# Kernel optimization log

Measured on AMD Instinct MI355X. Metric: run time of the kernel, lower is better.

## Reference

```python
import jax, jax.numpy as jnp
import numpy as np

THRESHOLD = 1e-3  # hardcoded `thresholds = 0.001` in the sparse branch


def setup_inputs() -> dict:
    key = jax.random.key(0)
    k1, k2, k3, k4, k5 = jax.random.split(key, 5)
    b, r, d_in, d_out = 8, 4096, 768, 768
    x = jax.random.normal(k1, (b, r, d_in), dtype=jnp.float32)
    weight = jax.random.normal(k2, (d_out, d_in), dtype=jnp.float32) * 0.02
    bias = jax.random.normal(k3, (d_out,), dtype=jnp.float32) * 0.02
    U = jax.random.normal(k4, (d_in, d_in), dtype=jnp.float32) * (d_in ** -0.5)
    VT = jax.random.normal(k5, (d_out, d_out), dtype=jnp.float32) * (d_out ** -0.5)
    return {"x": x, "weight": weight, "bias": bias, "U": U, "VT": VT}


def reference(x, weight, bias, U, VT):
    # Sparse path (len_grads >= 30) of LinearFunctionSparseGrad.forward.
    # h = x @ U.T, rotated into the gradient basis.  [b, r, c]
    h = jnp.einsum('brc,dc->brd', x, U)
    # Threshold-sparsify: zero entries with |h| <= 0.001.
    h = jnp.where(jnp.abs(h) > THRESHOLD, h, jnp.zeros((), h.dtype))
    # Original: gather nonzero rows/cols, h[rows][:, cols] @ weight.T[cols],
    # then scatter back via I[:, rows] @ res_. Dropped cols are exactly-zero
    # columns and dropped rows are exactly-zero rows, so the math equals a
    # dense matmul on the masked tensor (no [b*r, b*r] identity needed).
    res = jnp.einsum('brc,oc->bro', h, weight)        # h @ weight.T
    res = jnp.einsum('bro,po->brp', res, VT)          # res_ @ VT.T (self.VT=VT_orig.T => VT here)
    return res + bias
```

## Files before the change

### kernel.cpp

```cpp
#include <hip/hip_runtime.h>
#include <hip/hip_bf16.h>

typedef __bf16 bf16_t;
typedef bf16_t bf16x8 __attribute__((ext_vector_type(8)));
typedef bf16_t bf16x4 __attribute__((ext_vector_type(4)));
typedef float  f32x4  __attribute__((ext_vector_type(4)));

#define BM 256
#define BN 128
#define BK 32
#define ABUF (BM * BK)
#define BBUF (BN * BK)

enum { EPI_NONE = 0, EPI_THRESH = 1, EPI_BIAS = 2 };

__device__ __forceinline__ void memfence() { asm volatile("" ::: "memory"); }
__device__ __forceinline__ void blockbar() {
    memfence(); __builtin_amdgcn_s_barrier(); memfence();
}

#define GLD16(src, dst) __builtin_amdgcn_global_load_lds( \
    (const __attribute__((address_space(1))) void*)(src), \
    (__attribute__((address_space(3))) void*)(dst), 16, 0, 0)

template <int EPI, typename CT>
__device__ __forceinline__
void gemm_tile(const bf16_t* __restrict__ A, const bf16_t* __restrict__ B,
               CT* __restrict__ C, const float* __restrict__ bias,
               int m0, int n0, int N, int K,
               bf16_t* __restrict__ As, bf16_t* __restrict__ Bs)
{
    const int lane = threadIdx.x & 63;
    const int wave = threadIdx.x >> 6;
    const int wm = wave >> 1;
    const int wn = wave & 1;

    const int fm   = lane & 15;
    const int q    = lane >> 4;
    const int fsw2 = (fm ^ (fm >> 2)) & 3;

    const int NT = K / BK;

    const bf16_t* ga0; const bf16_t* ga1; const bf16_t* gb;
    {
        const int u0 = (wave * 2) * 64 + lane;
        const int r0 = u0 >> 2;
        ga0 = A + (size_t)(m0 + r0) * K + (((u0 & 3) ^ ((r0 ^ (r0 >> 2)) & 3)) * 8);
        const int u1 = (wave * 2 + 1) * 64 + lane;
        const int r1 = u1 >> 2;
        ga1 = A + (size_t)(m0 + r1) * K + (((u1 & 3) ^ ((r1 ^ (r1 >> 2)) & 3)) * 8);
        const int ub = wave * 64 + lane;
        const int rb = ub >> 2;
        gb  = B + (size_t)(n0 + rb) * K + (((ub & 3) ^ ((rb ^ (rb >> 2)) & 3)) * 8);
    }
    const int la0 = wave * 1024;
    const int la1 = wave * 1024 + 512;
    const int lb  = wave * 512;

#define STAGE(tt, Ad, Bd) do {                                   \
    GLD16(ga0 + (size_t)(tt) * BK, (Ad) + la0);                  \
    GLD16(ga1 + (size_t)(tt) * BK, (Ad) + la1);                  \
    GLD16(gb  + (size_t)(tt) * BK, (Bd) + lb);                   \
} while (0)

    f32x4 acc[4][4];
#pragma unroll
    for (int i = 0; i < 4; ++i)
#pragma unroll
        for (int j = 0; j < 4; ++j) acc[i][j] = (f32x4){0.f, 0.f, 0.f, 0.f};

    STAGE(0, As, Bs);
    STAGE(1, As + ABUF, Bs + BBUF);
    asm volatile("s_waitcnt vmcnt(3)" ::: "memory");
    blockbar();

    int bc = 0;
    for (int t = 0; t < NT; ++t) {
        const bf16_t* __restrict__ Ab = As + bc * ABUF;
        const bf16_t* __restrict__ Bb = Bs + bc * BBUF;
        const int bs2 = (bc >= 1) ? bc - 1 : 2;
        const bool do_stage = (t + 2 < NT);

        bf16x8 af[4], bfr[4];
#pragma unroll
        for (int i = 0; i < 4; ++i) {
            const int row = wm * 64 + i * 16 + fm;
            af[i] = *(const bf16x8*)(Ab + (size_t)(row * 4 + (q ^ fsw2)) * 8);
        }
#pragma unroll
        for (int j = 0; j < 4; ++j) {
            const int row = wn * 64 + j * 16 + fm;
            bfr[j] = *(const bf16x8*)(Bb + (size_t)(row * 4 + (q ^ fsw2)) * 8);
        }
        if (do_stage) STAGE(t + 2, As + bs2 * ABUF, Bs + bs2 * BBUF);

        __builtin_amdgcn_s_setprio(1);
#pragma unroll
        for (int i = 0; i < 4; ++i)
#pragma unroll
            for (int j = 0; j < 4; ++j)
                acc[i][j] = __builtin_amdgcn_mfma_f32_16x16x32_bf16(
                    af[i], bfr[j], acc[i][j], 0, 0, 0);
        __builtin_amdgcn_s_setprio(0);

        if (t < NT - 1) {
            asm volatile("s_waitcnt lgkmcnt(0)" ::: "memory");
            if (do_stage) asm volatile("s_waitcnt vmcnt(3)" ::: "memory");
            else          asm volatile("s_waitcnt vmcnt(0)" ::: "memory");
            blockbar();
        }
        bc = (bc >= 2) ? 0 : bc + 1;
    }

#pragma unroll
    for (int i = 0; i < 4; ++i) {
#pragma unroll
        for (int j = 0; j < 4; ++j) {
            const int col = n0 + wn * 64 + j * 16 + fm;
            float bv = 0.f;
            if (EPI == EPI_BIAS) bv = bias[col];
#pragma unroll
            for (int r = 0; r < 4; ++r) {
                const int row = m0 + wm * 64 + i * 16 + q * 4 + r;
                float v = acc[i][j][r];
                if (EPI == EPI_THRESH) v = (fabsf(v) > 1e-3f) ? v : 0.f;
                if (EPI == EPI_BIAS) v += bv;
                C[(size_t)row * N + col] = (CT)v;
            }
        }
    }
#undef STAGE
}

__global__ __launch_bounds__(512, 4)
void gemm_h_wc(const bf16_t* __restrict__ xb, const bf16_t* __restrict__ Ub,
               bf16_t* __restrict__ h,
               const bf16_t* __restrict__ VTb, const bf16_t* __restrict__ Wt,
               bf16_t* __restrict__ Wc)
{
    __shared__ __align__(16) bf16_t As[3 * ABUF];
    __shared__ __align__(16) bf16_t Bs[3 * BBUF];
    const int b = blockIdx.x;
    if (b < 18) {
        gemm_tile<EPI_NONE, bf16_t>(VTb, Wt, Wc, nullptr,
                                    (b / 6) * BM, (b % 6) * BN, 768, 768, As, Bs);
    } else {
        const int bb = b - 18;
        const int L = (bb & 7) * 96 + (bb >> 3);
        gemm_tile<EPI_THRESH, bf16_t>(xb, Ub, h, nullptr,
                                      (L / 6) * BM, (L % 6) * BN, 768, 768, As, Bs);
    }
}

__global__ __launch_bounds__(512, 4)
void gemm_out(const bf16_t* __restrict__ h, const bf16_t* __restrict__ Wc,
              float* __restrict__ out, const float* __restrict__ bias)
{
    __shared__ __align__(16) bf16_t As[3 * ABUF];
    __shared__ __align__(16) bf16_t Bs[3 * BBUF];
    const int b = blockIdx.x;
    const int L = (b & 7) * 96 + (b >> 3);
    gemm_tile<EPI_BIAS, float>(h, Wc, out, bias,
                               (L / 6) * BM, (L % 6) * BN, 768, 768, As, Bs);
}

__global__ __launch_bounds__(256)
void prep(const float* __restrict__ x, const float* __restrict__ U,
          const float* __restrict__ VT, const float* __restrict__ w,
          bf16_t* __restrict__ xb, bf16_t* __restrict__ Ub,
          bf16_t* __restrict__ VTb, bf16_t* __restrict__ Wt)
{
    __shared__ float tt[32][33];
    const int b = blockIdx.x;
    if (b < 12864) {
        const float* src; bf16_t* dst; size_t e;
        if (b < 12288)      { src = x;  dst = xb;  e = (size_t)b * 2048; }
        else if (b < 12576) { src = U;  dst = Ub;  e = (size_t)(b - 12288) * 2048; }
        else                { src = VT; dst = VTb; e = (size_t)(b - 12576) * 2048; }
        const size_t i = e + (size_t)threadIdx.x * 8;
        const f32x4 v0 = *(const f32x4*)(src + i);
        const f32x4 v1 = *(const f32x4*)(src + i + 4);
        bf16x8 o;
        o[0] = (bf16_t)v0[0]; o[1] = (bf16_t)v0[1];
        o[2] = (bf16_t)v0[2]; o[3] = (bf16_t)v0[3];
        o[4] = (bf16_t)v1[0]; o[5] = (bf16_t)v1[1];
        o[6] = (bf16_t)v1[2]; o[7] = (bf16_t)v1[3];
        *(bf16x8*)(dst + i) = o;
    } else {
        const int t = b - 12864;
        const int bx = (t % 24) * 32, by = (t / 24) * 32;
        const int tx = threadIdx.x & 31, ty = threadIdx.x >> 5;
#pragma unroll
        for (int i = 0; i < 32; i += 8)
            tt[ty + i][tx] = w[(size_t)(by + ty + i) * 768 + bx + tx];
        __syncthreads();
#pragma unroll
        for (int i = 0; i < 32; i += 8)
            Wt[(size_t)(bx + ty + i) * 768 + by + tx] = (bf16_t)tt[tx][ty + i];
    }
}

extern "C" void kernel_launch(void* const* d_in, const int* in_sizes, int n_in,
                              void* d_out, int out_size, void* d_ws, size_t ws_size,
                              hipStream_t stream)
{
    const float* x    = (const float*)d_in[0];
    const float* w    = (const float*)d_in[1];
    const float* bias = (const float*)d_in[2];
    const float* U    = (const float*)d_in[3];
    const float* VT   = (const float*)d_in[4];
    float* out = (float*)d_out;

    const int D = 768;
    const int M = 8 * 4096;
    const size_t MD = (size_t)M * D;
    const size_t DD = (size_t)D * D;

    char* ws = (char*)d_ws;
    bf16_t* xb  = (bf16_t*)ws;
    bf16_t* h   = (bf16_t*)(ws + MD * 2);
    bf16_t* Ub  = (bf16_t*)(ws + MD * 4);
    bf16_t* VTb = (bf16_t*)(ws + MD * 4 + DD * 2);
    bf16_t* Wt  = (bf16_t*)(ws + MD * 4 + DD * 4);
    bf16_t* Wc  = (bf16_t*)(ws + MD * 4 + DD * 6);

    prep<<<13440, 256, 0, stream>>>(x, U, VT, w, xb, Ub, VTb, Wt);
    gemm_h_wc<<<18 + 768, 512, 0, stream>>>(xb, Ub, h, VTb, Wt, Wc);
    gemm_out<<<768, 512, 0, stream>>>(h, Wc, out, bias);
}
```

Before: 278.0 us.

## Fuse fp32-to-bf16 conversion of x into the first GEMM's LDS load path

Drops the separate prep pass that turned x into a bf16 copy. The first GEMM now streams fp32 x tiles straight into LDS and converts them to bf16 while loading MFMA fragments. This removes one full fp32 read plus a bf16 write and re-read of the large activation tensor. In exchange the A tile in LDS doubles in size (80KB of shared memory), the pipeline drops from three stages to two with full vmcnt(0) waits, and occupancy may fall.

Result: slower. 289.7 us (+4.2%).

```diff
diff --git a/kernel.cpp b/kernel.cpp
--- a/kernel.cpp
+++ b/kernel.cpp
@@ -132,23 +132,142 @@
 #undef STAGE
 }
 
+template <int EPI>
+__device__ __forceinline__
+void gemm_h_af32(const float* __restrict__ A, const bf16_t* __restrict__ B,
+                 bf16_t* __restrict__ C, int m0, int n0, int N, int K,
+                 float* __restrict__ As, bf16_t* __restrict__ Bs)
+{
+    const int lane = threadIdx.x & 63;
+    const int wave = threadIdx.x >> 6;
+    const int wm = wave >> 1;
+    const int wn = wave & 1;
+
+    const int fm   = lane & 15;
+    const int q    = lane >> 4;
+    const int fsw  = fm & 7;
+    const int fsw2 = (fm ^ (fm >> 2)) & 3;
+
+    const int NT = K / BK;
+
+    const float* gA0; const float* gA1; const float* gA2; const float* gA3;
+    {
+        const int u0 = (wave * 4 + 0) * 64 + lane; const int r0 = u0 >> 3;
+        gA0 = A + (size_t)(m0 + r0) * K + ((u0 & 7) ^ (r0 & 7)) * 4;
+        const int u1 = (wave * 4 + 1) * 64 + lane; const int r1 = u1 >> 3;
+        gA1 = A + (size_t)(m0 + r1) * K + ((u1 & 7) ^ (r1 & 7)) * 4;
+        const int u2 = (wave * 4 + 2) * 64 + lane; const int r2 = u2 >> 3;
+        gA2 = A + (size_t)(m0 + r2) * K + ((u2 & 7) ^ (r2 & 7)) * 4;
+        const int u3 = (wave * 4 + 3) * 64 + lane; const int r3 = u3 >> 3;
+        gA3 = A + (size_t)(m0 + r3) * K + ((u3 & 7) ^ (r3 & 7)) * 4;
+    }
+    const bf16_t* gb;
+    {
+        const int ub = wave * 64 + lane;
+        const int rb = ub >> 2;
+        gb = B + (size_t)(n0 + rb) * K + (((ub & 3) ^ ((rb ^ (rb >> 2)) & 3)) * 8);
+    }
+    const int lA = wave * 1024;
+    const int lb = wave * 512;
+
+#define HSTAGE(tt, Ad, Bd) do {                                  \
+    GLD16(gA0 + (size_t)(tt) * BK, (Ad) + lA);                   \
+    GLD16(gA1 + (size_t)(tt) * BK, (Ad) + lA + 256);             \
+    GLD16(gA2 + (size_t)(tt) * BK, (Ad) + lA + 512);             \
+    GLD16(gA3 + (size_t)(tt) * BK, (Ad) + lA + 768);             \
+    GLD16(gb  + (size_t)(tt) * BK, (Bd) + lb);                   \
+} while (0)
+
+    f32x4 acc[4][4];
+#pragma unroll
+    for (int i = 0; i < 4; ++i)
+#pragma unroll
+        for (int j = 0; j < 4; ++j) acc[i][j] = (f32x4){0.f, 0.f, 0.f, 0.f};
+
+    HSTAGE(0, As, Bs);
+    asm volatile("s_waitcnt vmcnt(0)" ::: "memory");
+    blockbar();
+
+    for (int t = 0; t < NT; ++t) {
+        const float*  __restrict__ Ab = As + (t & 1) * (BM * BK);
+        const bf16_t* __restrict__ Bb = Bs + (t & 1) * BBUF;
+
+        if (t + 1 < NT)
+            HSTAGE(t + 1, As + ((t + 1) & 1) * (BM * BK),
+                          Bs + ((t + 1) & 1) * BBUF);
+
+        bf16x8 af[4], bfr[4];
+#pragma unroll
+        for (int i = 0; i < 4; ++i) {
+            const int row = wm * 64 + i * 16 + fm;
+            const f32x4 lo = *(const f32x4*)(Ab + (size_t)(row * 8 + ((2 * q)     ^ fsw)) * 4);
+            const f32x4 hi = *(const f32x4*)(Ab + (size_t)(row * 8 + ((2 * q + 1) ^ fsw)) * 4);
+            bf16x8 v;
+            v[0] = (bf16_t)lo[0]; v[1] = (bf16_t)lo[1];
+            v[2] = (bf16_t)lo[2]; v[3] = (bf16_t)lo[3];
+            v[4] = (bf16_t)hi[0]; v[5] = (bf16_t)hi[1];
+            v[6] = (bf16_t)hi[2]; v[7] = (bf16_t)hi[3];
+            af[i] = v;
+        }
+#pragma unroll
+        for (int j = 0; j < 4; ++j) {
+            const int row = wn * 64 + j * 16 + fm;
+            bfr[j] = *(const bf16x8*)(Bb + (size_t)(row * 4 + (q ^ fsw2)) * 8);
+        }
+
+        __builtin_amdgcn_s_setprio(1);
+#pragma unroll
+        for (int i = 0; i < 4; ++i)
+#pragma unroll
+            for (int j = 0; j < 4; ++j)
+                acc[i][j] = __builtin_amdgcn_mfma_f32_16x16x32_bf16(
+                    af[i], bfr[j], acc[i][j], 0, 0, 0);
+        __builtin_amdgcn_s_setprio(0);
+
+        if (t < NT - 1) {
+            asm volatile("s_waitcnt lgkmcnt(0)" ::: "memory");
+            asm volatile("s_waitcnt vmcnt(0)" ::: "memory");
+            blockbar();
+        }
+    }
+
+#pragma unroll
+    for (int i = 0; i < 4; ++i) {
+#pragma unroll
+        for (int j = 0; j < 4; ++j) {
+            const int col = n0 + wn * 64 + j * 16 + fm;
+#pragma unroll
+            for (int r = 0; r < 4; ++r) {
+                const int row = m0 + wm * 64 + i * 16 + q * 4 + r;
+                float v = acc[i][j][r];
+                if (EPI == EPI_THRESH) v = (fabsf(v) > 1e-3f) ? v : 0.f;
+                C[(size_t)row * N + col] = (bf16_t)v;
+            }
+        }
+    }
+#undef HSTAGE
+}
+
 __global__ __launch_bounds__(512, 4)
-void gemm_h_wc(const bf16_t* __restrict__ xb, const bf16_t* __restrict__ Ub,
+void gemm_h_wc(const float* __restrict__ x, const bf16_t* __restrict__ Ub,
                bf16_t* __restrict__ h,
                const bf16_t* __restrict__ VTb, const bf16_t* __restrict__ Wt,
                bf16_t* __restrict__ Wc)
 {
-    __shared__ __align__(16) bf16_t As[3 * ABUF];
-    __shared__ __align__(16) bf16_t Bs[3 * BBUF];
+    __shared__ __align__(16) char lds[81920];
     const int b = blockIdx.x;
     if (b < 18) {
+        bf16_t* As = (bf16_t*)lds;
+        bf16_t* Bs = (bf16_t*)(lds + 49152);
         gemm_tile<EPI_NONE, bf16_t>(VTb, Wt, Wc, nullptr,
                                     (b / 6) * BM, (b % 6) * BN, 768, 768, As, Bs);
     } else {
+        float*  As = (float*)lds;
+        bf16_t* Bs = (bf16_t*)(lds + 65536);
         const int bb = b - 18;
         const int L = (bb & 7) * 96 + (bb >> 3);
-        gemm_tile<EPI_THRESH, bf16_t>(xb, Ub, h, nullptr,
-                                      (L / 6) * BM, (L % 6) * BN, 768, 768, As, Bs);
+        gemm_h_af32<EPI_THRESH>(x, Ub, h,
+                                (L / 6) * BM, (L % 6) * BN, 768, 768, As, Bs);
     }
 }
 
@@ -165,18 +284,17 @@
 }
 
 __global__ __launch_bounds__(256)
-void prep(const float* __restrict__ x, const float* __restrict__ U,
-          const float* __restrict__ VT, const float* __restrict__ w,
-          bf16_t* __restrict__ xb, bf16_t* __restrict__ Ub,
-          bf16_t* __restrict__ VTb, bf16_t* __restrict__ Wt)
+void prep(const float* __restrict__ U, const float* __restrict__ VT,
+          const float* __restrict__ w,
+          bf16_t* __restrict__ Ub, bf16_t* __restrict__ VTb,
+          bf16_t* __restrict__ Wt)
 {
     __shared__ float tt[32][33];
     const int b = blockIdx.x;
-    if (b < 12864) {
+    if (b < 576) {
         const float* src; bf16_t* dst; size_t e;
-        if (b < 12288)      { src = x;  dst = xb;  e = (size_t)b * 2048; }
-        else if (b < 12576) { src = U;  dst = Ub;  e = (size_t)(b - 12288) * 2048; }
-        else                { src = VT; dst = VTb; e = (size_t)(b - 12576) * 2048; }
+        if (b < 288) { src = U;  dst = Ub;  e = (size_t)b * 2048; }
+        else         { src = VT; dst = VTb; e = (size_t)(b - 288) * 2048; }
         const size_t i = e + (size_t)threadIdx.x * 8;
         const f32x4 v0 = *(const f32x4*)(src + i);
         const f32x4 v1 = *(const f32x4*)(src + i + 4);
@@ -187,7 +305,7 @@
         o[6] = (bf16_t)v1[2]; o[7] = (bf16_t)v1[3];
         *(bf16x8*)(dst + i) = o;
     } else {
-        const int t = b - 12864;
+        const int t = b - 576;
         const int bx = (t % 24) * 32, by = (t / 24) * 32;
         const int tx = threadIdx.x & 31, ty = threadIdx.x >> 5;
 #pragma unroll
@@ -217,14 +335,13 @@
     const size_t DD = (size_t)D * D;
 
     char* ws = (char*)d_ws;
-    bf16_t* xb  = (bf16_t*)ws;
-    bf16_t* h   = (bf16_t*)(ws + MD * 2);
-    bf16_t* Ub  = (bf16_t*)(ws + MD * 4);
-    bf16_t* VTb = (bf16_t*)(ws + MD * 4 + DD * 2);
-    bf16_t* Wt  = (bf16_t*)(ws + MD * 4 + DD * 4);
-    bf16_t* Wc  = (bf16_t*)(ws + MD * 4 + DD * 6);
-
-    prep<<<13440, 256, 0, stream>>>(x, U, VT, w, xb, Ub, VTb, Wt);
-    gemm_h_wc<<<18 + 768, 512, 0, stream>>>(xb, Ub, h, VTb, Wt, Wc);
+    bf16_t* h   = (bf16_t*)ws;
+    bf16_t* Ub  = (bf16_t*)(ws + MD * 2);
+    bf16_t* VTb = (bf16_t*)(ws + MD * 2 + DD * 2);
+    bf16_t* Wt  = (bf16_t*)(ws + MD * 2 + DD * 4);
+    bf16_t* Wc  = (bf16_t*)(ws + MD * 2 + DD * 6);
+
+    prep<<<1152, 256, 0, stream>>>(U, VT, w, Ub, VTb, Wt);
+    gemm_h_wc<<<18 + 768, 512, 0, stream>>>(x, Ub, h, VTb, Wt, Wc);
     gemm_out<<<768, 512, 0, stream>>>(h, Wc, out, bias);
 }
```
